# Kernel tuning notes

Measured on AMD Instinct MI355X. Metric: run time of the kernel, lower is better.

## Reference

```python
import jax, jax.numpy as jnp
import numpy as np

N = 50000        # bs * n_node
E = 800000       # n_edge
INPUT_NF = 64
HIDDEN_NF = 64
N_CHANNEL = 4
D = 3            # spatial dim
EDGE_D = 16
EPS = 1e-12      # F.normalize clamp


def _unif(k, shape, fan_in):
    s = 1.0 / np.sqrt(fan_in)
    return jax.random.uniform(k, shape, jnp.float32, -s, s)


def setup_inputs() -> dict:
    key = jax.random.key(0)
    ks = jax.random.split(key, 12)
    h = jax.random.normal(ks[0], (N, INPUT_NF), jnp.float32)
    coord = jax.random.normal(ks[1], (N, N_CHANNEL, D), jnp.float32)
    row = jax.random.randint(ks[2], (E,), 0, N)
    col = jax.random.randint(ks[3], (E,), 0, N)
    edge_attr = jax.random.normal(ks[4], (E, EDGE_D), jnp.float32)
    kv_in = INPUT_NF + N_CHANNEL * N_CHANNEL + EDGE_D
    Wq = _unif(ks[5], (INPUT_NF, HIDDEN_NF), INPUT_NF)
    bq = _unif(ks[6], (HIDDEN_NF,), INPUT_NF)
    Wkv = _unif(ks[7], (kv_in, 2 * HIDDEN_NF), kv_in)
    bkv = _unif(ks[8], (2 * HIDDEN_NF,), kv_in)
    W1 = _unif(ks[9], (HIDDEN_NF, HIDDEN_NF), HIDDEN_NF)
    b1 = _unif(ks[10], (HIDDEN_NF,), HIDDEN_NF)
    # xavier_uniform with gain=0.001, no bias
    lim = 0.001 * np.sqrt(6.0 / (HIDDEN_NF + N_CHANNEL))
    W2 = jax.random.uniform(ks[11], (HIDDEN_NF, N_CHANNEL), jnp.float32, -lim, lim)
    return dict(h=h, coord=coord, row=row, col=col, edge_attr=edge_attr,
                Wq=Wq, bq=bq, Wkv=Wkv, bkv=bkv, W1=W1, b1=b1, W2=W2)


def reference(h, coord, edge_attr, Wq, bq, Wkv, bkv, W1, b1, W2, row, col):
    n_node = h.shape[0]
    # coord2radial
    coord_diff = coord[row] - coord[col]                                # [E,C,D]
    radial = jnp.einsum('ecd,efd->ecf', coord_diff, coord_diff)         # [E,C,C]
    # F.normalize(radial, dim=0): L2-normalize across the edge dimension
    norm = jnp.maximum(jnp.sqrt(jnp.sum(radial * radial, axis=0, keepdims=True)), EPS)
    radial = radial / norm
    # att_model
    q = h[row] @ Wq + bq                                                # [E,H]
    target_feat = jnp.concatenate(
        [radial.reshape(radial.shape[0], -1), h[col], edge_attr], axis=1)
    kv = target_feat @ Wkv + bkv                                        # [E,2H]
    k, v = kv[:, 0::2], kv[:, 1::2]                                     # [E,H] each
    alpha = jnp.sum(q * k, axis=1)                                      # [E]
    # scatter_softmax over segments given by row (numerically stable)
    seg_max = jax.ops.segment_max(alpha, row, num_segments=n_node)
    ex = jnp.exp(alpha - seg_max[row])
    seg_sum = jax.ops.segment_sum(ex, row, num_segments=n_node)
    att = ex / seg_sum[row]                                             # [E]
    # node_model (dropout in eval mode = identity)
    h_out = h + jax.ops.segment_sum(att[:, None] * v, row, num_segments=n_node)
    # coord_model: coord_mlp = Linear -> SiLU -> Linear(no bias)
    coord_v = att[:, None] * (jax.nn.silu(v @ W1 + b1) @ W2)            # [E,C]
    trans = coord_diff * coord_v[:, :, None]                            # [E,C,D]
    coord_out = coord + jax.ops.segment_sum(trans, row, num_segments=n_node)
    return h_out, coord_out, att
```

## Files before the change

### kernel.cpp

```cpp
#include <hip/hip_runtime.h>
#include <math.h>

#define NN 50000
#define NE 800000
#define NPREB 1024

typedef __attribute__((ext_vector_type(8))) short short8;
typedef __attribute__((ext_vector_type(4))) float floatx4;

__device__ __forceinline__ unsigned short bf16_of(float x) {
  unsigned u = __float_as_uint(x);
  u += 0x7fffu + ((u >> 16) & 1u);
  return (unsigned short)(u >> 16);
}
__device__ __forceinline__ float bf2f(unsigned short u) {
  return __uint_as_float(((unsigned)u) << 16);
}
__device__ __forceinline__ unsigned pack_bf(float a, float b) {
  unsigned ua = __float_as_uint(a); ua += 0x7fffu + ((ua >> 16) & 1u);
  unsigned ub = __float_as_uint(b); ub += 0x7fffu + ((ub >> 16) & 1u);
  return (ua >> 16) | (ub & 0xffff0000u);
}
__device__ __forceinline__ float blo(unsigned w) { return __uint_as_float(w << 16); }
__device__ __forceinline__ float bhi(unsigned w) { return __uint_as_float(w & 0xffff0000u); }

__global__ __launch_bounds__(256)
void k_pre(const float* __restrict__ coord, const int* __restrict__ row,
           const int* __restrict__ col, const float* __restrict__ Wkv,
           const float* __restrict__ W1, const float* __restrict__ Wq,
           float* __restrict__ norm_part, int* __restrict__ deg,
           unsigned short* __restrict__ Bkvb, unsigned short* __restrict__ W1tb,
           unsigned* __restrict__ Wqp) {
  __shared__ float nred[4][16];
  const int gid = blockIdx.x * 256 + threadIdx.x;
  const int np = gridDim.x * 256;
  for (int idx = gid; idx < 128 * 96; idx += np) {
    int n = idx & 127, kk = idx >> 7;
    float w = (n < 64) ? Wkv[kk * 128 + 2 * n] : Wkv[kk * 128 + 2 * (n - 64) + 1];
    Bkvb[n * 104 + kk] = bf16_of(w);
  }
  for (int idx = gid; idx < 64 * 64; idx += np) {
    int n = idx & 63, kk = idx >> 6;
    W1tb[n * 88 + kk] = bf16_of(W1[kk * 64 + n]);
  }
  for (int idx = gid; idx < 32 * 64; idx += np) {
    int i2 = idx >> 6, j = idx & 63;
    Wqp[idx] = pack_bf(Wq[(2 * i2) * 64 + j], Wq[(2 * i2 + 1) * 64 + j]);
  }
  const int lane = threadIdx.x & 63;
  const int grp = lane >> 4, g = lane & 15;
  const int c4 = g >> 2, f4 = g & 3;
  const int wid = blockIdx.x * 4 + (threadIdx.x >> 6);
  const int nw = gridDim.x * 4;
  float acc = 0.f;
  for (int base = wid * 4; base < NE; base += nw * 4) {
    int e = base + grp;
    int r = row[e], c = col[e];
    float cd = 0.f;
    if (g < 12) cd = coord[r * 12 + g] - coord[c * 12 + g];
    float rad = 0.f;
#pragma unroll
    for (int d = 0; d < 3; ++d)
      rad += __shfl(cd, grp * 16 + c4 * 3 + d) * __shfl(cd, grp * 16 + f4 * 3 + d);
    acc += rad * rad;
    if (g == 0) atomicAdd(deg + r, 1);
  }
  acc += __shfl_xor(acc, 16);
  acc += __shfl_xor(acc, 32);
  if (lane < 16) nred[threadIdx.x >> 6][lane] = acc;
  __syncthreads();
  if (threadIdx.x < 16) {
    float s = nred[0][threadIdx.x] + nred[1][threadIdx.x] +
              nred[2][threadIdx.x] + nred[3][threadIdx.x];
    norm_part[blockIdx.x * 16 + threadIdx.x] = s;
  }
}

__global__ __launch_bounds__(1024)
void k_scanq(const int* __restrict__ deg, int* __restrict__ startA,
             int* __restrict__ cursor, const float* __restrict__ norm_part,
             float* __restrict__ rnorm, const float* __restrict__ h,
             const unsigned* __restrict__ Wqp, const float* __restrict__ bq,
             unsigned short* __restrict__ qg2, unsigned short* __restrict__ hb) {
  __shared__ int part[1024];
  __shared__ float nr[64][16];
  __shared__ unsigned sWqp[32 * 64];
  __shared__ float sHr[16][64];
  const int t = threadIdx.x;
  if (blockIdx.x == 0) {
    {
      const int i = t >> 4, c = t & 15;
      float s = 0.f;
#pragma unroll
      for (int j = 0; j < 16; ++j) s += norm_part[((i + 64 * j) << 4) + c];
      nr[i][c] = s;
    }
    __syncthreads();
    if (t < 16) {
      float s = 0.f;
#pragma unroll 8
      for (int i = 0; i < 64; ++i) s += nr[i][t];
      rnorm[t] = 1.0f / fmaxf(sqrtf(s), 1e-12f);
    }
    const int CH = (NN + 1023) / 1024;
    const int lo = t * CH, hi = (lo + CH < NN) ? lo + CH : NN;
    int s = 0;
    for (int i = lo; i < hi; ++i) s += deg[i];
    part[t] = s;
    __syncthreads();
    for (int off = 1; off < 1024; off <<= 1) {
      int v = (t >= off) ? part[t - off] : 0;
      __syncthreads();
      part[t] += v;
      __syncthreads();
    }
    int base = (t == 0) ? 0 : part[t - 1];
    for (int i = lo; i < hi; ++i) {
      startA[i] = base; cursor[i] = base; base += deg[i];
    }
    if (t == 1023) startA[NN] = base;
    return;
  }
  for (int idx = t; idx < 2048; idx += 1024) sWqp[idx] = Wqp[idx];
  __syncthreads();
  const int wv = t >> 6, lane = t & 63;
  const int node = (blockIdx.x - 1) * 16 + wv;
  float hv = h[(size_t)node * 64 + lane];
  sHr[wv][lane] = hv;
  hb[(size_t)node * 64 + lane] = bf16_of(hv);
  float q = bq[lane];
  const float2* hp = (const float2*)sHr[wv];
#pragma unroll 8
  for (int i2 = 0; i2 < 32; ++i2) {
    unsigned w = sWqp[i2 * 64 + lane];
    float2 hbv = hp[i2];
    q += hbv.x * blo(w) + hbv.y * bhi(w);
  }
  qg2[(size_t)node * 64 + (lane & 15) * 4 + (lane >> 4)] = bf16_of(q);
}

__global__ void k_scatter(const int* __restrict__ row, const int* __restrict__ col,
                          const float* __restrict__ edge_attr,
                          int* __restrict__ cursor, int* __restrict__ iperm,
                          unsigned* __restrict__ rcp, uint4* __restrict__ eab) {
  int e = blockIdx.x * 256 + threadIdx.x;
  if (e < NE) {
    int r = row[e], c = col[e];
    int p = atomicAdd(cursor + r, 1);
    iperm[e] = p;
    rcp[p] = ((unsigned)r << 16) | (unsigned)c;
    const float4* ep = (const float4*)(edge_attr + (size_t)e * 16);
    float4 f0 = ep[0], f1 = ep[1], f2 = ep[2], f3 = ep[3];
    uint4 a, b;
    a.x = pack_bf(f0.x, f0.y); a.y = pack_bf(f0.z, f0.w);
    a.z = pack_bf(f1.x, f1.y); a.w = pack_bf(f1.z, f1.w);
    b.x = pack_bf(f2.x, f2.y); b.y = pack_bf(f2.z, f2.w);
    b.z = pack_bf(f3.x, f3.y); b.w = pack_bf(f3.z, f3.w);
    eab[(size_t)p * 2]     = a;
    eab[(size_t)p * 2 + 1] = b;
  }
}

__global__ __launch_bounds__(512, 6)
void k_kv(const unsigned short* __restrict__ hb, const float* __restrict__ coord,
          const float* __restrict__ edge_unused, const float* __restrict__ bkv,
          const float* __restrict__ b1, const float* __restrict__ W2,
          const float* __restrict__ rnorm, const unsigned* __restrict__ rcp,
          const uint4* __restrict__ eab,
          const unsigned short* __restrict__ Bkvb,
          const unsigned short* __restrict__ W1tb,
          const unsigned short* __restrict__ qg2,
          float* __restrict__ exg, float* __restrict__ l_g,
          float* __restrict__ hacc_g, float* __restrict__ cacc_g) {
  __shared__ __align__(16) unsigned short sA[128][104];
  __shared__ __align__(16) unsigned short sB[128][104];
  __shared__ unsigned sRC[128];
  unsigned short (*sW1t)[88] = (unsigned short (*)[88])&sB[0][0];

  const int tid = threadIdx.x;
  const int base = blockIdx.x * 128;

  const uint4* gw = (const uint4*)W1tb;
  uint4 w1a = gw[tid];
  uint4 w1b;
  if (tid < 192) w1b = gw[512 + tid];

  if (tid < 128) sRC[tid] = rcp[base + tid];
  if (tid < 256) {
    int s = tid >> 1;
    *(uint4*)&sA[s][80 + (tid & 1) * 8] = eab[(size_t)base * 2 + tid];
  }
  {
    const uint4* gb = (const uint4*)Bkvb;
    uint4* sb = (uint4*)&sB[0][0];
    for (int idx = tid; idx < 1664; idx += 512) sb[idx] = gb[idx];
  }
  __syncthreads();

  for (int idx = tid; idx < 1024; idx += 512) {
    int s = idx >> 3, k8 = idx & 7;
    unsigned c = sRC[s] & 0xffffu;
    uint4 u = ((const uint4*)(hb + (size_t)c * 64))[k8];
    *(uint4*)&sA[s][16 + k8 * 8] = u;
  }
  const int wv = tid >> 6, lane = tid & 63;
  float cdp[4];
  {
    const int grp = lane >> 4, g = lane & 15;
    const int c4 = g >> 2, f4 = g & 3;
    const float rn = rnorm[g];
#pragma unroll
    for (int it = 0; it < 4; ++it) {
      int slot = 16 * wv + it * 4 + grp;
      unsigned rc = sRC[slot];
      int r = (int)(rc >> 16), c = (int)(rc & 0xffffu);
      float cd = 0.f;
      if (g < 12) cd = coord[r * 12 + g] - coord[c * 12 + g];
      cdp[it] = cd;
      float rad = 0.f;
#pragma unroll
      for (int d = 0; d < 3; ++d)
        rad += __shfl(cd, grp * 16 + c4 * 3 + d) * __shfl(cd, grp * 16 + f4 * 3 + d);
      sA[slot][g] = bf16_of(rad * rn);
    }
  }
  __syncthreads();

  const int m16 = lane & 15, quad = lane >> 4;
  const int arow = 16 * wv + m16;

  floatx4 acc[8];
#pragma unroll
  for (int i = 0; i < 8; ++i) acc[i] = (floatx4){0.f, 0.f, 0.f, 0.f};
#pragma unroll
  for (int ks = 0; ks < 3; ++ks) {
    short8 af = *(const short8*)&sA[arow][ks * 32 + quad * 8];
#pragma unroll
    for (int nt = 0; nt < 8; ++nt) {
      short8 bf = *(const short8*)&sB[nt * 16 + m16][ks * 32 + quad * 8];
      acc[nt] = __builtin_amdgcn_mfma_f32_16x16x32_bf16(af, bf, acc[nt], 0, 0, 0);
    }
  }
#pragma unroll
  for (int nt = 0; nt < 4; ++nt) {
    float bk = bkv[2 * (m16 + 16 * nt)];
    float bv = bkv[2 * (m16 + 16 * nt) + 1];
#pragma unroll
    for (int r = 0; r < 4; ++r) { acc[nt][r] += bk; acc[nt + 4][r] += bv; }
  }
  float part[4] = {0.f, 0.f, 0.f, 0.f};
#pragma unroll
  for (int r = 0; r < 4; ++r) {
    unsigned nrow = sRC[16 * wv + quad * 4 + r] >> 16;
    uint2 qp = *(const uint2*)(qg2 + (size_t)nrow * 64 + m16 * 4);
    part[r] += blo(qp.x) * acc[0][r] + bhi(qp.x) * acc[1][r] +
               blo(qp.y) * acc[2][r] + bhi(qp.y) * acc[3][r];
  }
#pragma unroll
  for (int off = 1; off < 16; off <<= 1) {
#pragma unroll
    for (int r = 0; r < 4; ++r) part[r] += __shfl_xor(part[r], off);
  }
  float ex[4];
#pragma unroll
  for (int r = 0; r < 4; ++r) ex[r] = __expf(part[r]);
  if (m16 == 0) {
#pragma unroll
    for (int r = 0; r < 4; ++r)
      exg[base + 16 * wv + quad * 4 + r] = ex[r];
  }
#pragma unroll
  for (int nt = 0; nt < 4; ++nt)
#pragma unroll
    for (int r = 0; r < 4; ++r)
      sA[16 * wv + quad * 4 + r][m16 + 16 * nt] = bf16_of(acc[4 + nt][r]);
#pragma unroll
  for (int it = 0; it < 4; ++it)
    if (m16 < 12) sA[16 * wv + it * 4 + quad][64 + m16] = bf16_of(cdp[it]);

  __syncthreads();
  {
    unsigned short* sw = &sB[0][0];
    *(uint4*)&sw[(size_t)tid * 8] = w1a;
    if (tid < 192) *(uint4*)&sw[(size_t)(512 + tid) * 8] = w1b;
  }
  __syncthreads();

  floatx4 tacc[4];
#pragma unroll
  for (int i = 0; i < 4; ++i) tacc[i] = (floatx4){0.f, 0.f, 0.f, 0.f};
#pragma unroll
  for (int ks = 0; ks < 2; ++ks) {
    short8 af = *(const short8*)&sA[arow][ks * 32 + quad * 8];
#pragma unroll
    for (int nt = 0; nt < 4; ++nt) {
      short8 bf = *(const short8*)&sW1t[nt * 16 + m16][ks * 32 + quad * 8];
      tacc[nt] = __builtin_amdgcn_mfma_f32_16x16x32_bf16(af, bf, tacc[nt], 0, 0, 0);
    }
  }
#pragma unroll
  for (int nt = 0; nt < 4; ++nt) {
    float bb = b1[m16 + 16 * nt];
#pragma unroll
    for (int r = 0; r < 4; ++r) {
      float t = tacc[nt][r] + bb;
      tacc[nt][r] = t * __builtin_amdgcn_rcpf(1.f + __expf(-t));
    }
  }
  float w0[16];
#pragma unroll
  for (int r = 0; r < 4; ++r)
#pragma unroll
    for (int c = 0; c < 4; ++c) w0[r * 4 + c] = 0.f;
#pragma unroll
  for (int nt = 0; nt < 4; ++nt) {
    float4 w2r = ((const float4*)W2)[m16 + 16 * nt];
#pragma unroll
    for (int r = 0; r < 4; ++r) {
      w0[r * 4 + 0] += tacc[nt][r] * w2r.x;
      w0[r * 4 + 1] += tacc[nt][r] * w2r.y;
      w0[r * 4 + 2] += tacc[nt][r] * w2r.z;
      w0[r * 4 + 3] += tacc[nt][r] * w2r.w;
    }
  }
  float rs1[8];
#pragma unroll
  for (int jj = 0; jj < 8; ++jj) {
    float snd = (m16 & 8) ? w0[jj] : w0[jj + 8];
    float rcv = __shfl_xor(snd, 8);
    rs1[jj] = ((m16 & 8) ? w0[jj + 8] : w0[jj]) + rcv;
  }
  float rs2[4];
#pragma unroll
  for (int jj = 0; jj < 4; ++jj) {
    float snd = (m16 & 4) ? rs1[jj] : rs1[jj + 4];
    float rcv = __shfl_xor(snd, 4);
    rs2[jj] = ((m16 & 4) ? rs1[jj + 4] : rs1[jj]) + rcv;
  }
  float rs3[2];
#pragma unroll
  for (int jj = 0; jj < 2; ++jj) {
    float snd = (m16 & 2) ? rs2[jj] : rs2[jj + 2];
    float rcv = __shfl_xor(snd, 2);
    rs3[jj] = ((m16 & 2) ? rs2[jj + 2] : rs2[jj]) + rcv;
  }
  float cvtot;
  {
    float snd = (m16 & 1) ? rs3[0] : rs3[1];
    float rcv = __shfl_xor(snd, 1);
    cvtot = ((m16 & 1) ? rs3[1] : rs3[0]) + rcv;
  }
  const int d3 = (m16 < 12) ? ((m16 * 11) >> 5) : 3;
  float tr[4];
#pragma unroll
  for (int r = 0; r < 4; ++r) {
    float cvv = __shfl(cvtot, (quad << 4) + r * 4 + d3);
    tr[r] = (m16 < 12) ? bf2f(sA[16 * wv + quad * 4 + r][64 + m16]) * cvv : 0.f;
  }

  int s = 0;
  while (s < 16) {
    int n = (int)(sRC[16 * wv + s] >> 16);
    int e2 = s + 1;
    while (e2 < 16 && (int)(sRC[16 * wv + e2] >> 16) == n) ++e2;
    float hp0 = 0.f, hp1 = 0.f, hp2 = 0.f, hp3 = 0.f, lp = 0.f, cp = 0.f;
#pragma unroll
    for (int r = 0; r < 4; ++r) {
      int rowi = quad * 4 + r;
      float w = (rowi >= s && rowi < e2) ? ex[r] : 0.f;
      hp0 += w * acc[4][r];
      hp1 += w * acc[5][r];
      hp2 += w * acc[6][r];
      hp3 += w * acc[7][r];
      lp  += (rowi >= s && rowi < e2) ? ex[r] : 0.f;
      cp  += w * tr[r];
    }
    hp0 += __shfl_xor(hp0, 16); hp0 += __shfl_xor(hp0, 32);
    hp1 += __shfl_xor(hp1, 16); hp1 += __shfl_xor(hp1, 32);
    hp2 += __shfl_xor(hp2, 16); hp2 += __shfl_xor(hp2, 32);
    hp3 += __shfl_xor(hp3, 16); hp3 += __shfl_xor(hp3, 32);
    lp  += __shfl_xor(lp, 16);  lp  += __shfl_xor(lp, 32);
    cp  += __shfl_xor(cp, 16);  cp  += __shfl_xor(cp, 32);
    if (quad == 0) {
      float* hg = hacc_g + (size_t)n * 64;
      atomicAdd(hg + m16,      hp0);
      atomicAdd(hg + m16 + 16, hp1);
      atomicAdd(hg + m16 + 32, hp2);
      atomicAdd(hg + m16 + 48, hp3);
      if (m16 < 12) atomicAdd(cacc_g + (size_t)n * 12 + m16, cp);
      if (m16 == 0) atomicAdd(l_g + n, lp);
    }
    s = e2;
  }
}

__global__ __launch_bounds__(256)
void k_fin(const float* __restrict__ h, const float* __restrict__ coord,
           const int* __restrict__ row, const int* __restrict__ iperm,
           const float* __restrict__ exg, const float* __restrict__ l_g,
           const float* __restrict__ hacc_g, const float* __restrict__ cacc_g,
           float* __restrict__ out) {
  const int wv = threadIdx.x >> 6, lane = threadIdx.x & 63;
  const int node = blockIdx.x * 4 + wv;
  const float l = l_g[node];
  const float inv = (l > 0.f) ? 1.f / l : 0.f;
  out[node * 64 + lane] =
      h[(size_t)node * 64 + lane] + hacc_g[(size_t)node * 64 + lane] * inv;
  if (lane < 12)
    out[NN * 64 + node * 12 + lane] =
        coord[node * 12 + lane] + cacc_g[(size_t)node * 12 + lane] * inv;
  const int e = blockIdx.x * 256 + threadIdx.x;
  if (e < NE) {
    float le = l_g[row[e]];
    out[NN * 64 + NN * 12 + e] = exg[iperm[e]] * __builtin_amdgcn_rcpf(le);
  }
}

extern "C" void kernel_launch(void* const* d_in, const int* in_sizes, int n_in,
                              void* d_out, int out_size, void* d_ws, size_t ws_size,
                              hipStream_t stream) {
  const float* h         = (const float*)d_in[0];
  const float* coord     = (const float*)d_in[1];
  const int*   row       = (const int*)d_in[2];
  const int*   col       = (const int*)d_in[3];
  const float* edge_attr = (const float*)d_in[4];
  const float* Wq        = (const float*)d_in[5];
  const float* bq        = (const float*)d_in[6];
  const float* Wkv       = (const float*)d_in[7];
  const float* bkv       = (const float*)d_in[8];
  const float* W1        = (const float*)d_in[9];
  const float* b1        = (const float*)d_in[10];
  const float* W2        = (const float*)d_in[11];
  float* out = (float*)d_out;

  size_t off = 0;
  char* wsb = (char*)d_ws;
  auto alloc = [&](size_t bytes) {
    off = (off + 255) & ~(size_t)255;
    void* p = wsb + off; off += bytes; return p;
  };
  int*            deg      = (int*)alloc((size_t)NN * 4);
  float*          l_g      = (float*)alloc((size_t)NN * 4);
  float*          hacc_g   = (float*)alloc((size_t)NN * 64 * 4);
  float*          cacc_g   = (float*)alloc((size_t)NN * 12 * 4);
  size_t zbytes = off;
  float*          norm_part= (float*)alloc((size_t)NPREB * 16 * 4);
  float*          rnorm    = (float*)alloc(16 * 4);
  int*            startA   = (int*)alloc(((size_t)NN + 1) * 4);
  int*            cursor   = (int*)alloc((size_t)NN * 4);
  unsigned*       rcp      = (unsigned*)alloc((size_t)NE * 4);
  int*            iperm    = (int*)alloc((size_t)NE * 4);
  float*          exg      = (float*)alloc((size_t)NE * 4);
  uint4*          eab      = (uint4*)alloc((size_t)NE * 32);
  unsigned short* qg2      = (unsigned short*)alloc((size_t)NN * 64 * 2);
  unsigned short* hb       = (unsigned short*)alloc((size_t)NN * 64 * 2);
  unsigned short* Bkvb     = (unsigned short*)alloc(128 * 104 * 2);
  unsigned short* W1tb     = (unsigned short*)alloc(64 * 88 * 2);
  unsigned*       Wqp      = (unsigned*)alloc(32 * 64 * 4);

  hipMemsetAsync(d_ws, 0, zbytes, stream);

  k_pre<<<NPREB, 256, 0, stream>>>(coord, row, col, Wkv, W1, Wq,
                                   norm_part, deg, Bkvb, W1tb, Wqp);
  k_scanq<<<1 + NN / 16, 1024, 0, stream>>>(deg, startA, cursor, norm_part,
                                            rnorm, h, Wqp, bq, qg2, hb);
  k_scatter<<<(NE + 255) / 256, 256, 0, stream>>>(row, col, edge_attr, cursor,
                                                  iperm, rcp, eab);
  k_kv<<<NE / 128, 512, 0, stream>>>(hb, coord, edge_attr, bkv, b1, W2,
                                     rnorm, rcp, eab, Bkvb, W1tb, qg2,
                                     exg, l_g, hacc_g, cacc_g);
  k_fin<<<NN / 4, 256, 0, stream>>>(h, coord, row, iperm, exg, l_g,
                                    hacc_g, cacc_g, out);
}
```

Baseline: 486.1 us.

## Precompute radial and coord diffs in scatter into per-edge packed records

Moves the coord_diff gather and radial feature computation from the main kv kernel into the scatter kernel. Scatter now writes a 64-byte bf16 record per sorted edge holding normalized radial, coord diffs and the packed row/col. The kv kernel loads these records with one coalesced read instead of gathering coord and using shuffles, and keeps coord diffs in a separate shared region. This trades extra global write/read traffic (64 B per edge) for fewer random gathers and less work in k_kv. Coord diffs are now rounded to bf16 before use, as they were before.

```diff
diff --git a/kernel.cpp b/kernel.cpp
--- a/kernel.cpp
+++ b/kernel.cpp
@@ -141,14 +141,16 @@
 
 __global__ void k_scatter(const int* __restrict__ row, const int* __restrict__ col,
                           const float* __restrict__ edge_attr,
+                          const float* __restrict__ coord,
+                          const float* __restrict__ rnorm,
                           int* __restrict__ cursor, int* __restrict__ iperm,
-                          unsigned* __restrict__ rcp, uint4* __restrict__ eab) {
+                          uint4* __restrict__ rec, uint4* __restrict__ eab) {
   int e = blockIdx.x * 256 + threadIdx.x;
-  if (e < NE) {
-    int r = row[e], c = col[e];
-    int p = atomicAdd(cursor + r, 1);
-    iperm[e] = p;
-    rcp[p] = ((unsigned)r << 16) | (unsigned)c;
+  if (e >= NE) return;
+  int r = row[e], c = col[e];
+  int p = atomicAdd(cursor + r, 1);
+  iperm[e] = p;
+  {
     const float4* ep = (const float4*)(edge_attr + (size_t)e * 16);
     float4 f0 = ep[0], f1 = ep[1], f2 = ep[2], f3 = ep[3];
     uint4 a, b;
@@ -159,14 +161,54 @@
     eab[(size_t)p * 2]     = a;
     eab[(size_t)p * 2 + 1] = b;
   }
+  float cd[12];
+  {
+    const float4* cr = (const float4*)(coord + (size_t)r * 12);
+    const float4* cc = (const float4*)(coord + (size_t)c * 12);
+#pragma unroll
+    for (int q = 0; q < 3; ++q) {
+      float4 a = cr[q], b = cc[q];
+      cd[q * 4 + 0] = a.x - b.x; cd[q * 4 + 1] = a.y - b.y;
+      cd[q * 4 + 2] = a.z - b.z; cd[q * 4 + 3] = a.w - b.w;
+    }
+  }
+  float rn[16];
+  {
+    const float4* rp = (const float4*)rnorm;
+#pragma unroll
+    for (int q = 0; q < 4; ++q) {
+      float4 v = rp[q];
+      rn[q * 4] = v.x; rn[q * 4 + 1] = v.y; rn[q * 4 + 2] = v.z; rn[q * 4 + 3] = v.w;
+    }
+  }
+  unsigned rw[8];
+#pragma unroll
+  for (int g = 0; g < 16; g += 2) {
+    int c40 = g >> 2, f40 = g & 3;
+    int c41 = (g + 1) >> 2, f41 = (g + 1) & 3;
+    float v0 = cd[c40 * 3] * cd[f40 * 3] + cd[c40 * 3 + 1] * cd[f40 * 3 + 1] +
+               cd[c40 * 3 + 2] * cd[f40 * 3 + 2];
+    float v1 = cd[c41 * 3] * cd[f41 * 3] + cd[c41 * 3 + 1] * cd[f41 * 3 + 1] +
+               cd[c41 * 3 + 2] * cd[f41 * 3 + 2];
+    rw[g >> 1] = pack_bf(v0 * rn[g], v1 * rn[g + 1]);
+  }
+  unsigned cw[6];
+#pragma unroll
+  for (int w = 0; w < 6; ++w) cw[w] = pack_bf(cd[2 * w], cd[2 * w + 1]);
+  uint4* rp4 = rec + (size_t)p * 4;
+  uint4 q0, q1, q2, q3;
+  q0.x = rw[0]; q0.y = rw[1]; q0.z = rw[2]; q0.w = rw[3];
+  q1.x = rw[4]; q1.y = rw[5]; q1.z = rw[6]; q1.w = rw[7];
+  q2.x = cw[0]; q2.y = cw[1]; q2.z = cw[2]; q2.w = cw[3];
+  q3.x = cw[4]; q3.y = cw[5]; q3.z = ((unsigned)r << 16) | (unsigned)c; q3.w = 0;
+  rp4[0] = q0; rp4[1] = q1; rp4[2] = q2; rp4[3] = q3;
 }
 
 __global__ __launch_bounds__(512, 6)
-void k_kv(const unsigned short* __restrict__ hb, const float* __restrict__ coord,
-          const float* __restrict__ edge_unused, const float* __restrict__ bkv,
-          const float* __restrict__ b1, const float* __restrict__ W2,
-          const float* __restrict__ rnorm, const unsigned* __restrict__ rcp,
-          const uint4* __restrict__ eab,
+void k_kv(const unsigned short* __restrict__ hb,
+          const uint4* __restrict__ rec, const uint4* __restrict__ eab,
+          const float* __restrict__ bkv, const float* __restrict__ b1,
+          const float* __restrict__ W2,
           const unsigned short* __restrict__ Bkvb,
           const unsigned short* __restrict__ W1tb,
           const unsigned short* __restrict__ qg2,
@@ -176,6 +218,8 @@
   __shared__ __align__(16) unsigned short sB[128][104];
   __shared__ unsigned sRC[128];
   unsigned short (*sW1t)[88] = (unsigned short (*)[88])&sB[0][0];
+  unsigned short (*sCD)[16] =
+      (unsigned short (*)[16])((char*)&sB[0][0] + 64 * 88 * 2);
 
   const int tid = threadIdx.x;
   const int base = blockIdx.x * 128;
@@ -185,7 +229,12 @@
   uint4 w1b;
   if (tid < 192) w1b = gw[512 + tid];
 
-  if (tid < 128) sRC[tid] = rcp[base + tid];
+  uint4 rw = rec[(size_t)base * 4 + tid];
+  const int rs = tid >> 2, rj = tid & 3;
+  if (rj == 0)      *(uint4*)&sA[rs][0] = rw;
+  else if (rj == 1) *(uint4*)&sA[rs][8] = rw;
+  else if (rj == 3) sRC[rs] = rw.z;
+
   if (tid < 256) {
     int s = tid >> 1;
     *(uint4*)&sA[s][80 + (tid & 1) * 8] = eab[(size_t)base * 2 + tid];
@@ -203,29 +252,9 @@
     uint4 u = ((const uint4*)(hb + (size_t)c * 64))[k8];
     *(uint4*)&sA[s][16 + k8 * 8] = u;
   }
+  __syncthreads();
+
   const int wv = tid >> 6, lane = tid & 63;
-  float cdp[4];
-  {
-    const int grp = lane >> 4, g = lane & 15;
-    const int c4 = g >> 2, f4 = g & 3;
-    const float rn = rnorm[g];
-#pragma unroll
-    for (int it = 0; it < 4; ++it) {
-      int slot = 16 * wv + it * 4 + grp;
-      unsigned rc = sRC[slot];
-      int r = (int)(rc >> 16), c = (int)(rc & 0xffffu);
-      float cd = 0.f;
-      if (g < 12) cd = coord[r * 12 + g] - coord[c * 12 + g];
-      cdp[it] = cd;
-      float rad = 0.f;
-#pragma unroll
-      for (int d = 0; d < 3; ++d)
-        rad += __shfl(cd, grp * 16 + c4 * 3 + d) * __shfl(cd, grp * 16 + f4 * 3 + d);
-      sA[slot][g] = bf16_of(rad * rn);
-    }
-  }
-  __syncthreads();
-
   const int m16 = lane & 15, quad = lane >> 4;
   const int arow = 16 * wv + m16;
 
@@ -274,15 +303,17 @@
 #pragma unroll
     for (int r = 0; r < 4; ++r)
       sA[16 * wv + quad * 4 + r][m16 + 16 * nt] = bf16_of(acc[4 + nt][r]);
-#pragma unroll
-  for (int it = 0; it < 4; ++it)
-    if (m16 < 12) sA[16 * wv + it * 4 + quad][64 + m16] = bf16_of(cdp[it]);
 
   __syncthreads();
   {
     unsigned short* sw = &sB[0][0];
     *(uint4*)&sw[(size_t)tid * 8] = w1a;
     if (tid < 192) *(uint4*)&sw[(size_t)(512 + tid) * 8] = w1b;
+    if (rj == 2) *(uint4*)&sCD[rs][0] = rw;
+    else if (rj == 3) {
+      uint2 t2; t2.x = rw.x; t2.y = rw.y;
+      *(uint2*)&sCD[rs][8] = t2;
+    }
   }
   __syncthreads();
 
@@ -355,7 +386,7 @@
 #pragma unroll
   for (int r = 0; r < 4; ++r) {
     float cvv = __shfl(cvtot, (quad << 4) + r * 4 + d3);
-    tr[r] = (m16 < 12) ? bf2f(sA[16 * wv + quad * 4 + r][64 + m16]) * cvv : 0.f;
+    tr[r] = (m16 < 12) ? bf2f(sCD[16 * wv + quad * 4 + r][m16]) * cvv : 0.f;
   }
 
   int s = 0;
@@ -448,9 +479,9 @@
   float*          rnorm    = (float*)alloc(16 * 4);
   int*            startA   = (int*)alloc(((size_t)NN + 1) * 4);
   int*            cursor   = (int*)alloc((size_t)NN * 4);
-  unsigned*       rcp      = (unsigned*)alloc((size_t)NE * 4);
   int*            iperm    = (int*)alloc((size_t)NE * 4);
   float*          exg      = (float*)alloc((size_t)NE * 4);
+  uint4*          rec      = (uint4*)alloc((size_t)NE * 64);
   uint4*          eab      = (uint4*)alloc((size_t)NE * 32);
   unsigned short* qg2      = (unsigned short*)alloc((size_t)NN * 64 * 2);
   unsigned short* hb       = (unsigned short*)alloc((size_t)NN * 64 * 2);
@@ -464,10 +495,10 @@
                                    norm_part, deg, Bkvb, W1tb, Wqp);
   k_scanq<<<1 + NN / 16, 1024, 0, stream>>>(deg, startA, cursor, norm_part,
                                             rnorm, h, Wqp, bq, qg2, hb);
-  k_scatter<<<(NE + 255) / 256, 256, 0, stream>>>(row, col, edge_attr, cursor,
-                                                  iperm, rcp, eab);
-  k_kv<<<NE / 128, 512, 0, stream>>>(hb, coord, edge_attr, bkv, b1, W2,
-                                     rnorm, rcp, eab, Bkvb, W1tb, qg2,
+  k_scatter<<<(NE + 255) / 256, 256, 0, stream>>>(row, col, edge_attr, coord,
+                                                  rnorm, cursor, iperm, rec, eab);
+  k_kv<<<NE / 128, 512, 0, stream>>>(hb, rec, eab, bkv, b1, W2,
+                                     Bkvb, W1tb, qg2,
                                      exg, l_g, hacc_g, cacc_g);
   k_fin<<<NN / 4, 256, 0, stream>>>(h, coord, row, iperm, exg, l_g,
                                     hacc_g, cacc_g, out);
```

New measurement: 508.1 us. +4.5%, slower.
